# Kernel tuning notes

Hardware: AMD Instinct MI355X
Metric: run time of the kernel (lower is better)

Reference implementation:

```python
import jax, jax.numpy as jnp
import numpy as np

EPS = 1e-10
B, N, F, H, C = 4, 512, 64, 64, 32


def _lin_init(key, fan_in, fan_out):
    return jax.random.normal(key, (fan_in, fan_out), dtype=jnp.float32) / np.sqrt(fan_in)


def setup_inputs() -> dict:
    key = jax.random.key(0)
    ks = jax.random.split(key, 12)
    inp = {
        "h": jax.random.normal(ks[0], (B, N, F), dtype=jnp.float32),
        "x": jax.random.normal(ks[1], (B, N, 3), dtype=jnp.float32),
        "mask": jnp.ones((B, N, N), dtype=jnp.float32),
        # edge_model (ConcatenationFilter): Linear(2F+1,H) SiLU Linear(H,H) SiLU
        "We1": _lin_init(ks[2], 2 * F + 1, H), "be1": jnp.zeros((H,), jnp.float32),
        "We2": _lin_init(ks[3], H, H), "be2": jnp.zeros((H,), jnp.float32),
        # coefficients_mlp: Linear(H,H) SiLU Linear(H,C)
        "Wc1": _lin_init(ks[4], H, H), "bc1": jnp.zeros((H,), jnp.float32),
        "Wc2": _lin_init(ks[5], H, C), "bc2": jnp.zeros((C,), jnp.float32),
        # post_norm_mlp: Linear(C,H) SiLU Linear(H,H)
        "Wp1": _lin_init(ks[6], C, H), "bp1": jnp.zeros((H,), jnp.float32),
        "Wp2": _lin_init(ks[7], H, H), "bp2": jnp.zeros((H,), jnp.float32),
        # node_mlp: Linear(2H+F,H) SiLU Linear(H,F)
        "Wn1": _lin_init(ks[8], 2 * H + F, H), "bn1": jnp.zeros((H,), jnp.float32),
        "Wn2": _lin_init(ks[9], H, F), "bn2": jnp.zeros((F,), jnp.float32),
    }
    return inp


def _forward(h, x, mask, We1, be1, We2, be2, Wc1, bc1, Wc2, bc2,
             Wp1, bp1, Wp2, bp2, Wn1, bn1, Wn2, bn2):
    b, n, f = h.shape
    # pairwise displacements: entry (i, j) = x_j - x_i  -> [B,N,N,3]
    x_minus_xt = x[..., None, :, :] - x[..., :, None, :]
    # squared pairwise distance (norm with eps=0, then squared) -> [B,N,N,1]
    norm2 = jnp.sum(x_minus_xt * x_minus_xt, axis=-1, keepdims=True)
    # h_cat_ht: [h_i broadcast over j dim order per get_h_cat_h] -> [B,N,N,2F]
    hi = jnp.broadcast_to(h[..., None, :, :], (b, n, n, f))
    hj = jnp.broadcast_to(h[..., :, None, :], (b, n, n, f))
    edge_in = jnp.concatenate([hi, hj, norm2], axis=-1)  # [B,N,N,2F+1]
    # ConcatenationFilter edge model
    h_e_mtx = jax.nn.silu(jax.nn.silu(edge_in @ We1 + be1) @ We2 + be2)  # [B,N,N,H]
    # aggregate (masked sum over neighbor dim -2)
    h_e = jnp.sum(h_e_mtx * mask[..., None], axis=-2)  # [B,N,H]
    # spatial attention
    coeff = jax.nn.silu(h_e_mtx @ Wc1 + bc1) @ Wc2 + bc2  # [B,N,N,C]
    vec = x_minus_xt / (norm2 ** 2.0 + EPS)  # [B,N,N,3]
    # combinations = coeff[...,c,None] * vec[...,None,:]; masked sum over dim -3 (j)
    comb_sum = jnp.einsum("bijc,bijd,bij->bicd", coeff, vec, mask)  # [B,N,C,3]
    comb_norm = jnp.sum(comb_sum * comb_sum, axis=-1)  # [B,N,C]
    h_comb = jax.nn.silu(comb_norm @ Wp1 + bp1) @ Wp2 + bp2  # [B,N,H]
    # node model with residual
    node_in = jnp.concatenate([h, h_e, h_comb], axis=-1)  # [B,N,F+2H]
    out = jax.nn.silu(node_in @ Wn1 + bn1) @ Wn2 + bn2  # [B,N,F]
    h_new = h + out
    return h_new


def reference(h, x, mask, We1, be1, We2, be2, Wc1, bc1, Wc2, bc2,
              Wp1, bp1, Wp2, bp2, Wn1, bn1, Wn2, bn2):
    h_new = _forward(h, x, mask, We1, be1, We2, be2, Wc1, bc1, Wc2, bc2,
                     Wp1, bp1, Wp2, bp2, Wn1, bn1, Wn2, bn2)
    # update_coordinate=False: x passes through unchanged
    return (h_new, x)
```

## Files before the change

### kernel.cpp

```cpp
#include <hip/hip_runtime.h>

#define BB 4
#define NN 512
#define FF 64

typedef __attribute__((ext_vector_type(8))) short short8v;
typedef __attribute__((ext_vector_type(4))) float f32x4;

__device__ __forceinline__ float silu_f(float v) {
  return v * __builtin_amdgcn_rcpf(1.0f + __expf(-v));
}
__device__ __forceinline__ unsigned short f2bf(float f) {
  unsigned int u = __float_as_uint(f);
  unsigned int r = (u + 0x7FFFu + ((u >> 16) & 1u)) >> 16;
  return (unsigned short)r;
}
__device__ __forceinline__ float bf2f(unsigned short s) {
  return __uint_as_float(((unsigned int)s) << 16);
}
__device__ __forceinline__ unsigned cvt_pk_bf16(float a, float b) {
  unsigned r;
  asm("v_cvt_pk_bf16_f32 %0, %1, %2" : "=v"(r) : "v"(a), "v"(b));
  return r;
}

#define AIDX(j, k) ((((j) << 6)) | (((((k) >> 3) ^ ((j) & 7))) << 3) | ((k) & 7))

__global__ void sake_prep(const float* __restrict__ h, const float* __restrict__ We1,
                          const float* __restrict__ be1, const float* __restrict__ We2,
                          const float* __restrict__ Wc1, const float* __restrict__ Wc2,
                          float* __restrict__ G, float* __restrict__ Base,
                          unsigned short* __restrict__ w2h, unsigned short* __restrict__ w2l,
                          unsigned short* __restrict__ w3h, unsigned short* __restrict__ w3l,
                          unsigned short* __restrict__ w4h, unsigned short* __restrict__ w4l)
{
  const int wg = (int)blockIdx.x, tid = (int)threadIdx.x;
  if (wg < 64) {
    __shared__ float sH[32][64];
    const int r0 = wg * 32;
    for (int idx = tid; idx < 2048; idx += 256) sH[idx >> 6][idx & 63] = h[r0 * 64 + idx];
    __syncthreads();
    const int rl = tid >> 3;
    const int o0 = (tid & 7) * 8;
    float aG[8], aB[8];
    #pragma unroll
    for (int o = 0; o < 8; ++o) { aG[o] = 0.f; aB[o] = be1[o0 + o]; }
    for (int k = 0; k < 64; ++k) {
      const float hv = sH[rl][k];
      const float4 g0 = *(const float4*)&We1[k * 64 + o0];
      const float4 g1 = *(const float4*)&We1[k * 64 + o0 + 4];
      const float4 b0 = *(const float4*)&We1[(64 + k) * 64 + o0];
      const float4 b1 = *(const float4*)&We1[(64 + k) * 64 + o0 + 4];
      aG[0] = fmaf(hv, g0.x, aG[0]); aG[1] = fmaf(hv, g0.y, aG[1]);
      aG[2] = fmaf(hv, g0.z, aG[2]); aG[3] = fmaf(hv, g0.w, aG[3]);
      aG[4] = fmaf(hv, g1.x, aG[4]); aG[5] = fmaf(hv, g1.y, aG[5]);
      aG[6] = fmaf(hv, g1.z, aG[6]); aG[7] = fmaf(hv, g1.w, aG[7]);
      aB[0] = fmaf(hv, b0.x, aB[0]); aB[1] = fmaf(hv, b0.y, aB[1]);
      aB[2] = fmaf(hv, b0.z, aB[2]); aB[3] = fmaf(hv, b0.w, aB[3]);
      aB[4] = fmaf(hv, b1.x, aB[4]); aB[5] = fmaf(hv, b1.y, aB[5]);
      aB[6] = fmaf(hv, b1.z, aB[6]); aB[7] = fmaf(hv, b1.w, aB[7]);
    }
    const size_t base = (size_t)(r0 + rl) * 64 + o0;
    *(float4*)&G[base]        = make_float4(aG[0], aG[1], aG[2], aG[3]);
    *(float4*)&G[base + 4]    = make_float4(aG[4], aG[5], aG[6], aG[7]);
    *(float4*)&Base[base]     = make_float4(aB[0], aB[1], aB[2], aB[3]);
    *(float4*)&Base[base + 4] = make_float4(aB[4], aB[5], aB[6], aB[7]);
  } else {
    for (int idx = tid; idx < 10240; idx += 256) {
      float w; unsigned short *ph, *pl; int pos;
      if (idx < 4096)      { const int o = idx >> 6,          k = idx & 63;
                             w = We2[k * 64 + o]; ph = w2h; pl = w2l; pos = o * 64 + k; }
      else if (idx < 8192) { const int t = idx - 4096, o = t >> 6, k = t & 63;
                             w = Wc1[k * 64 + o]; ph = w3h; pl = w3l; pos = o * 64 + k; }
      else                 { const int t = idx - 8192, c = t >> 6, k = t & 63;
                             w = Wc2[k * 32 + c]; ph = w4h; pl = w4l; pos = c * 64 + k; }
      const unsigned short hi = f2bf(w);
      const unsigned short lo = f2bf(w - bf2f(hi));
      ph[pos] = hi; pl[pos] = lo;
    }
  }
}

__device__ __forceinline__ void pack_store4(unsigned short* sAh, int a,
                                            float v0, float v1, float v2, float v3) {
  *(uint2*)&sAh[a] = make_uint2(cvt_pk_bf16(v0, v1), cvt_pk_bf16(v2, v3));
}

__global__ __launch_bounds__(256, 3)
void sake_mfma(const float* __restrict__ h, const float* __restrict__ x,
               const float* __restrict__ mask,
               const float* __restrict__ We1, const float* __restrict__ be2,
               const float* __restrict__ bc1, const float* __restrict__ bc2,
               const float* __restrict__ Wp1, const float* __restrict__ bp1,
               const float* __restrict__ Wp2, const float* __restrict__ bp2,
               const float* __restrict__ Wn1, const float* __restrict__ bn1,
               const float* __restrict__ Wn2, const float* __restrict__ bn2,
               const float* __restrict__ G, const float* __restrict__ Base,
               const unsigned short* __restrict__ w2h, const unsigned short* __restrict__ w2l,
               const unsigned short* __restrict__ w3h, const unsigned short* __restrict__ w3l,
               const unsigned short* __restrict__ w4h, const unsigned short* __restrict__ w4l,
               float* __restrict__ out)
{
  __shared__ unsigned short sAh[2 * 4096];
  __shared__ float sVecM[64][4];
  __shared__ float sMask[64];
  __shared__ float sBase[64], sW1n[64], sHi[64], sXi[4];
  __shared__ float sHe[64], sCombP[4 * 48], sCN[32], sTmp[64], sHcomb[64];

  const int tid  = (int)threadIdx.x;
  const int blk  = (int)blockIdx.x;
  const int b    = blk >> 9;
  const int i    = blk & 511;
  const int lane = tid & 63;
  const int wid  = tid >> 6;
  const int l15  = lane & 15;
  const int lg   = lane >> 4;
  const int mb   = wid * 16;
  const int mb2  = (wid >> 1) * 16;

  if (tid < 64) {
    sBase[tid] = Base[((size_t)(b * NN + i)) * 64 + tid];
    sW1n[tid]  = We1[128 * 64 + tid];
    sHi[tid]   = h[((size_t)(b * NN + i)) * 64 + tid];
  }
  if (tid < 3) sXi[tid] = x[((size_t)(b * NN + i)) * 3 + tid];

  short8v w2hF[2], w2lF[2], w3hF[2], w3lF[2], w4hF[2], w4lF[2];
  #pragma unroll
  for (int ks = 0; ks < 2; ++ks) {
    const int ko = ks * 32 + lg * 8;
    w2hF[ks] = *(const short8v*)&w2h[(mb  + l15) * 64 + ko];
    w2lF[ks] = *(const short8v*)&w2l[(mb  + l15) * 64 + ko];
    w3hF[ks] = *(const short8v*)&w3h[(mb  + l15) * 64 + ko];
    w3lF[ks] = *(const short8v*)&w3l[(mb  + l15) * 64 + ko];
    w4hF[ks] = *(const short8v*)&w4h[(mb2 + l15) * 64 + ko];
    w4lF[ks] = *(const short8v*)&w4l[(mb2 + l15) * 64 + ko];
  }
  float be2v[4], bc1v[4], bc2v[4];
  #pragma unroll
  for (int r = 0; r < 4; ++r) {
    be2v[r] = be2[mb  + lg * 4 + r];
    bc1v[r] = bc1[mb  + lg * 4 + r];
    bc2v[r] = bc2[mb2 + lg * 4 + r];
  }

  float heAcc[4] = {0.f, 0.f, 0.f, 0.f};
  float cAcc[4][3] = {};

  for (int jt = 0; jt < 8; ++jt) {
    const int jb = jt * 64;
    __syncthreads();

    if (tid < 64) {
      const int j = tid;
      const size_t xo = ((size_t)(b * NN + jb + j)) * 3;
      const float dx = x[xo + 0] - sXi[0];
      const float dy = x[xo + 1] - sXi[1];
      const float dz = x[xo + 2] - sXi[2];
      const float n2 = dx * dx + dy * dy + dz * dz;
      const float inv = __builtin_amdgcn_rcpf(n2 * n2 + 1e-10f);
      const float m = mask[((size_t)(b * NN + i)) * NN + jb + j];
      sVecM[j][0] = dx * inv * m; sVecM[j][1] = dy * inv * m; sVecM[j][2] = dz * inv * m;
      sMask[j] = m;
    }

    {
      const int j = l15 + wid * 16;
      const int jglob = jb + j;
      const size_t xo = ((size_t)(b * NN + jglob)) * 3;
      const float dx = x[xo + 0] - sXi[0];
      const float dy = x[xo + 1] - sXi[1];
      const float dz = x[xo + 2] - sXi[2];
      const float n2 = dx * dx + dy * dy + dz * dz;
      #pragma unroll
      for (int kk = 0; kk < 4; ++kk) {
        const int kb = lg * 16 + kk * 4;
        const float4 g4 = *(const float4*)&G[((size_t)(b * NN + jglob)) * 64 + kb];
        const float4 bs = *(const float4*)&sBase[kb];
        const float4 wn = *(const float4*)&sW1n[kb];
        const float v0 = silu_f(g4.x + bs.x + n2 * wn.x);
        const float v1 = silu_f(g4.y + bs.y + n2 * wn.y);
        const float v2 = silu_f(g4.z + bs.z + n2 * wn.z);
        const float v3 = silu_f(g4.w + bs.w + n2 * wn.w);
        pack_store4(sAh, AIDX(j, kb), v0, v1, v2, v3);
      }
    }
    __syncthreads();

    #pragma unroll
    for (int nf = 0; nf < 4; ++nf) {
      const int jn = nf * 16 + l15;
      f32x4 acc = { be2v[0], be2v[1], be2v[2], be2v[3] };
      #pragma unroll
      for (int ks = 0; ks < 2; ++ks) {
        const int kb = ks * 32 + lg * 8;
        const short8v bh = *(const short8v*)&sAh[AIDX(jn, kb)];
        acc = __builtin_amdgcn_mfma_f32_16x16x32_bf16(w2hF[ks], bh, acc, 0, 0, 0);
        acc = __builtin_amdgcn_mfma_f32_16x16x32_bf16(w2lF[ks], bh, acc, 0, 0, 0);
      }
      const float m = sMask[jn];
      float v[4];
      #pragma unroll
      for (int r = 0; r < 4; ++r) { v[r] = silu_f(acc[r]); heAcc[r] = fmaf(v[r], m, heAcc[r]); }
      pack_store4(sAh, 4096 + AIDX(jn, mb + lg * 4), v[0], v[1], v[2], v[3]);
    }
    __syncthreads();

    #pragma unroll
    for (int nf = 0; nf < 4; ++nf) {
      const int jn = nf * 16 + l15;
      f32x4 acc = { bc1v[0], bc1v[1], bc1v[2], bc1v[3] };
      #pragma unroll
      for (int ks = 0; ks < 2; ++ks) {
        const int kb = ks * 32 + lg * 8;
        const short8v bh = *(const short8v*)&sAh[4096 + AIDX(jn, kb)];
        acc = __builtin_amdgcn_mfma_f32_16x16x32_bf16(w3hF[ks], bh, acc, 0, 0, 0);
        acc = __builtin_amdgcn_mfma_f32_16x16x32_bf16(w3lF[ks], bh, acc, 0, 0, 0);
      }
      float v[4];
      #pragma unroll
      for (int r = 0; r < 4; ++r) v[r] = silu_f(acc[r]);
      pack_store4(sAh, AIDX(jn, mb + lg * 4), v[0], v[1], v[2], v[3]);
    }
    __syncthreads();

    #pragma unroll
    for (int nf = 0; nf < 2; ++nf) {
      const int jn = (wid & 1) * 32 + nf * 16 + l15;
      f32x4 acc = { bc2v[0], bc2v[1], bc2v[2], bc2v[3] };
      #pragma unroll
      for (int ks = 0; ks < 2; ++ks) {
        const int kb = ks * 32 + lg * 8;
        const short8v bh = *(const short8v*)&sAh[AIDX(jn, kb)];
        acc = __builtin_amdgcn_mfma_f32_16x16x32_bf16(w4hF[ks], bh, acc, 0, 0, 0);
        acc = __builtin_amdgcn_mfma_f32_16x16x32_bf16(w4lF[ks], bh, acc, 0, 0, 0);
      }
      const float vm0 = sVecM[jn][0], vm1 = sVecM[jn][1], vm2 = sVecM[jn][2];
      #pragma unroll
      for (int r = 0; r < 4; ++r) {
        cAcc[r][0] = fmaf(acc[r], vm0, cAcc[r][0]);
        cAcc[r][1] = fmaf(acc[r], vm1, cAcc[r][1]);
        cAcc[r][2] = fmaf(acc[r], vm2, cAcc[r][2]);
      }
    }
  }

  #pragma unroll
  for (int r = 0; r < 4; ++r) {
    float s = heAcc[r];
    s += __shfl_xor(s, 1); s += __shfl_xor(s, 2); s += __shfl_xor(s, 4); s += __shfl_xor(s, 8);
    if (l15 == 0) sHe[mb + lg * 4 + r] = s;
  }
  #pragma unroll
  for (int r = 0; r < 4; ++r)
    #pragma unroll
    for (int d = 0; d < 3; ++d) {
      float s = cAcc[r][d];
      s += __shfl_xor(s, 1); s += __shfl_xor(s, 2); s += __shfl_xor(s, 4); s += __shfl_xor(s, 8);
      if (l15 == 0) sCombP[wid * 48 + (lg * 4 + r) * 3 + d] = s;
    }
  __syncthreads();
  if (tid < 32) {
    const int c = tid, w0 = (c >> 4) * 2, cl = c & 15;
    const float s0 = sCombP[w0 * 48 + cl * 3 + 0] + sCombP[(w0 + 1) * 48 + cl * 3 + 0];
    const float s1 = sCombP[w0 * 48 + cl * 3 + 1] + sCombP[(w0 + 1) * 48 + cl * 3 + 1];
    const float s2 = sCombP[w0 * 48 + cl * 3 + 2] + sCombP[(w0 + 1) * 48 + cl * 3 + 2];
    sCN[c] = s0 * s0 + s1 * s1 + s2 * s2;
  }
  __syncthreads();

  if (tid < 64) {
    float s = bp1[tid];
    #pragma unroll 8
    for (int c = 0; c < 32; ++c) s = fmaf(sCN[c], Wp1[c * 64 + tid], s);
    sTmp[tid] = silu_f(s);
  }
  __syncthreads();
  if (tid < 64) {
    float s = bp2[tid];
    #pragma unroll 16
    for (int k = 0; k < 64; ++k) s = fmaf(sTmp[k], Wp2[k * 64 + tid], s);
    sHcomb[tid] = s;
  }
  __syncthreads();
  if (tid < 64) {
    float s = bn1[tid];
    #pragma unroll 16
    for (int m = 0; m < 64; ++m) s = fmaf(sHi[m],    Wn1[m * 64 + tid],         s);
    #pragma unroll 16
    for (int m = 0; m < 64; ++m) s = fmaf(sHe[m],    Wn1[(64 + m) * 64 + tid],  s);
    #pragma unroll 16
    for (int m = 0; m < 64; ++m) s = fmaf(sHcomb[m], Wn1[(128 + m) * 64 + tid], s);
    sTmp[tid] = silu_f(s);
  }
  __syncthreads();
  if (tid < 64) {
    float s = bn2[tid];
    #pragma unroll 16
    for (int k = 0; k < 64; ++k) s = fmaf(sTmp[k], Wn2[k * 64 + tid], s);
    out[((size_t)(b * NN + i)) * 64 + tid] = sHi[tid] + s;
  } else if (tid < 67) {
    const int d = tid - 64;
    out[(size_t)BB * NN * FF + ((size_t)(b * NN + i)) * 3 + d] = x[((size_t)(b * NN + i)) * 3 + d];
  }
}

extern "C" void kernel_launch(void* const* d_in, const int* in_sizes, int n_in,
                              void* d_out, int out_size, void* d_ws, size_t ws_size,
                              hipStream_t stream) {
  const float* h    = (const float*)d_in[0];
  const float* x    = (const float*)d_in[1];
  const float* mask = (const float*)d_in[2];
  const float* We1  = (const float*)d_in[3];
  const float* be1  = (const float*)d_in[4];
  const float* We2  = (const float*)d_in[5];
  const float* be2  = (const float*)d_in[6];
  const float* Wc1  = (const float*)d_in[7];
  const float* bc1  = (const float*)d_in[8];
  const float* Wc2  = (const float*)d_in[9];
  const float* bc2  = (const float*)d_in[10];
  const float* Wp1  = (const float*)d_in[11];
  const float* bp1  = (const float*)d_in[12];
  const float* Wp2  = (const float*)d_in[13];
  const float* bp2  = (const float*)d_in[14];
  const float* Wn1  = (const float*)d_in[15];
  const float* bn1  = (const float*)d_in[16];
  const float* Wn2  = (const float*)d_in[17];
  const float* bn2  = (const float*)d_in[18];
  float* out = (float*)d_out;

  float* G    = (float*)d_ws;
  float* Base = G + 2048 * 64;
  unsigned short* w2h = (unsigned short*)(Base + 2048 * 64);
  unsigned short* w2l = w2h + 4096;
  unsigned short* w3h = w2l + 4096;
  unsigned short* w3l = w3h + 4096;
  unsigned short* w4h = w3l + 4096;
  unsigned short* w4l = w4h + 2048;

  hipLaunchKernelGGL(sake_prep, dim3(65), dim3(256), 0, stream,
                     h, We1, be1, We2, Wc1, Wc2, G, Base,
                     w2h, w2l, w3h, w3l, w4h, w4l);
  hipLaunchKernelGGL(sake_mfma, dim3(BB * NN), dim3(256), 0, stream,
                     h, x, mask, We1, be2, bc1, bc2,
                     Wp1, bp1, Wp2, bp2, Wn1, bn1, Wn2, bn2,
                     G, Base, w2h, w2l, w3h, w3l, w4h, w4l, out);
}
```

Baseline: 127.3 us.

## Process 128-neighbor tiles with triple-buffered LDS to cut barriers per tile

Doubles the neighbor tile from 64 to 128 (4 iterations instead of 8) and gives each MLP stage its own LDS buffer, so the loop-top barrier is dropped and there are three barriers per tile instead of four. The final coefficient layer is reorganized so each wave computes all 32 outputs for its own neighbor rows, keeping the displacement vectors in registers instead of a shared sVecM array. Biases move to shared memory. LDS use grows to about 48KB per block and register pressure rises, which may reduce occupancy under the 3-blocks-per-CU launch bound.

```diff
diff --git a/kernel.cpp b/kernel.cpp
--- a/kernel.cpp
+++ b/kernel.cpp
@@ -81,9 +81,9 @@
   }
 }
 
-__device__ __forceinline__ void pack_store4(unsigned short* sAh, int a,
+__device__ __forceinline__ void pack_store4(unsigned short* sA, int a,
                                             float v0, float v1, float v2, float v3) {
-  *(uint2*)&sAh[a] = make_uint2(cvt_pk_bf16(v0, v1), cvt_pk_bf16(v2, v3));
+  *(uint2*)&sA[a] = make_uint2(cvt_pk_bf16(v0, v1), cvt_pk_bf16(v2, v3));
 }
 
 __global__ __launch_bounds__(256, 3)
@@ -101,11 +101,11 @@
                const unsigned short* __restrict__ w4h, const unsigned short* __restrict__ w4l,
                float* __restrict__ out)
 {
-  __shared__ unsigned short sAh[2 * 4096];
-  __shared__ float sVecM[64][4];
-  __shared__ float sMask[64];
-  __shared__ float sBase[64], sW1n[64], sHi[64], sXi[4];
-  __shared__ float sHe[64], sCombP[4 * 48], sCN[32], sTmp[64], sHcomb[64];
+  __shared__ unsigned short sAct[3 * 8192];
+  __shared__ float sMaskL[128];
+  __shared__ float sBase[64], sW1n[64], sHi[64];
+  __shared__ float sB2[64], sB3[64], sB4[32];
+  __shared__ float sHe[64], sCombP[4][96], sCN[32], sTmp[64], sHcomb[64];
 
   const int tid  = (int)threadIdx.x;
   const int blk  = (int)blockIdx.x;
@@ -116,131 +116,135 @@
   const int l15  = lane & 15;
   const int lg   = lane >> 4;
   const int mb   = wid * 16;
-  const int mb2  = (wid >> 1) * 16;
 
   if (tid < 64) {
     sBase[tid] = Base[((size_t)(b * NN + i)) * 64 + tid];
     sW1n[tid]  = We1[128 * 64 + tid];
     sHi[tid]   = h[((size_t)(b * NN + i)) * 64 + tid];
-  }
-  if (tid < 3) sXi[tid] = x[((size_t)(b * NN + i)) * 3 + tid];
-
-  short8v w2hF[2], w2lF[2], w3hF[2], w3lF[2], w4hF[2], w4lF[2];
+    sB2[tid]   = be2[tid];
+    sB3[tid]   = bc1[tid];
+  }
+  if (tid < 32) sB4[tid] = bc2[tid];
+  const float xi0 = x[((size_t)(b * NN + i)) * 3 + 0];
+  const float xi1 = x[((size_t)(b * NN + i)) * 3 + 1];
+  const float xi2 = x[((size_t)(b * NN + i)) * 3 + 2];
+
+  short8v w2hF[2], w2lF[2], w3hF[2], w3lF[2], w4hF[2][2], w4lF[2][2];
   #pragma unroll
   for (int ks = 0; ks < 2; ++ks) {
     const int ko = ks * 32 + lg * 8;
-    w2hF[ks] = *(const short8v*)&w2h[(mb  + l15) * 64 + ko];
-    w2lF[ks] = *(const short8v*)&w2l[(mb  + l15) * 64 + ko];
-    w3hF[ks] = *(const short8v*)&w3h[(mb  + l15) * 64 + ko];
-    w3lF[ks] = *(const short8v*)&w3l[(mb  + l15) * 64 + ko];
-    w4hF[ks] = *(const short8v*)&w4h[(mb2 + l15) * 64 + ko];
-    w4lF[ks] = *(const short8v*)&w4l[(mb2 + l15) * 64 + ko];
-  }
-  float be2v[4], bc1v[4], bc2v[4];
-  #pragma unroll
-  for (int r = 0; r < 4; ++r) {
-    be2v[r] = be2[mb  + lg * 4 + r];
-    bc1v[r] = bc1[mb  + lg * 4 + r];
-    bc2v[r] = bc2[mb2 + lg * 4 + r];
+    w2hF[ks] = *(const short8v*)&w2h[(mb + l15) * 64 + ko];
+    w2lF[ks] = *(const short8v*)&w2l[(mb + l15) * 64 + ko];
+    w3hF[ks] = *(const short8v*)&w3h[(mb + l15) * 64 + ko];
+    w3lF[ks] = *(const short8v*)&w3l[(mb + l15) * 64 + ko];
+    #pragma unroll
+    for (int m2 = 0; m2 < 2; ++m2) {
+      w4hF[m2][ks] = *(const short8v*)&w4h[(m2 * 16 + l15) * 64 + ko];
+      w4lF[m2][ks] = *(const short8v*)&w4l[(m2 * 16 + l15) * 64 + ko];
+    }
   }
 
   float heAcc[4] = {0.f, 0.f, 0.f, 0.f};
-  float cAcc[4][3] = {};
-
-  for (int jt = 0; jt < 8; ++jt) {
-    const int jb = jt * 64;
-    __syncthreads();
-
-    if (tid < 64) {
-      const int j = tid;
-      const size_t xo = ((size_t)(b * NN + jb + j)) * 3;
-      const float dx = x[xo + 0] - sXi[0];
-      const float dy = x[xo + 1] - sXi[1];
-      const float dz = x[xo + 2] - sXi[2];
+  float cAcc[2][4][3] = {};
+
+  __syncthreads();
+
+  for (int jt = 0; jt < 4; ++jt) {
+    const int jb = jt * 128;
+
+    float vmr[2][3], n2v[2];
+    #pragma unroll
+    for (int jj = 0; jj < 2; ++jj) {
+      const int j = jb + jj * 64 + wid * 16 + l15;
+      const size_t xo = ((size_t)(b * NN + j)) * 3;
+      const float dx = x[xo + 0] - xi0;
+      const float dy = x[xo + 1] - xi1;
+      const float dz = x[xo + 2] - xi2;
       const float n2 = dx * dx + dy * dy + dz * dz;
       const float inv = __builtin_amdgcn_rcpf(n2 * n2 + 1e-10f);
-      const float m = mask[((size_t)(b * NN + i)) * NN + jb + j];
-      sVecM[j][0] = dx * inv * m; sVecM[j][1] = dy * inv * m; sVecM[j][2] = dz * inv * m;
-      sMask[j] = m;
-    }
-
-    {
-      const int j = l15 + wid * 16;
-      const int jglob = jb + j;
-      const size_t xo = ((size_t)(b * NN + jglob)) * 3;
-      const float dx = x[xo + 0] - sXi[0];
-      const float dy = x[xo + 1] - sXi[1];
-      const float dz = x[xo + 2] - sXi[2];
-      const float n2 = dx * dx + dy * dy + dz * dz;
-      #pragma unroll
-      for (int kk = 0; kk < 4; ++kk) {
-        const int kb = lg * 16 + kk * 4;
-        const float4 g4 = *(const float4*)&G[((size_t)(b * NN + jglob)) * 64 + kb];
-        const float4 bs = *(const float4*)&sBase[kb];
-        const float4 wn = *(const float4*)&sW1n[kb];
+      const float m = mask[((size_t)(b * NN + i)) * NN + j];
+      vmr[jj][0] = dx * inv * m; vmr[jj][1] = dy * inv * m; vmr[jj][2] = dz * inv * m;
+      n2v[jj] = n2;
+      if (lg == 0) sMaskL[jj * 64 + wid * 16 + l15] = m;
+    }
+    #pragma unroll
+    for (int kk = 0; kk < 4; ++kk) {
+      const int kb = lg * 16 + kk * 4;
+      const float4 bs = *(const float4*)&sBase[kb];
+      const float4 wn = *(const float4*)&sW1n[kb];
+      #pragma unroll
+      for (int jj = 0; jj < 2; ++jj) {
+        const int jloc = jj * 64 + wid * 16 + l15;
+        const float4 g4 = *(const float4*)&G[((size_t)(b * NN + jb + jloc)) * 64 + kb];
+        const float n2 = n2v[jj];
         const float v0 = silu_f(g4.x + bs.x + n2 * wn.x);
         const float v1 = silu_f(g4.y + bs.y + n2 * wn.y);
         const float v2 = silu_f(g4.z + bs.z + n2 * wn.z);
         const float v3 = silu_f(g4.w + bs.w + n2 * wn.w);
-        pack_store4(sAh, AIDX(j, kb), v0, v1, v2, v3);
+        pack_store4(sAct, AIDX(jloc, kb), v0, v1, v2, v3);
       }
     }
     __syncthreads();
 
-    #pragma unroll
-    for (int nf = 0; nf < 4; ++nf) {
-      const int jn = nf * 16 + l15;
-      f32x4 acc = { be2v[0], be2v[1], be2v[2], be2v[3] };
-      #pragma unroll
-      for (int ks = 0; ks < 2; ++ks) {
-        const int kb = ks * 32 + lg * 8;
-        const short8v bh = *(const short8v*)&sAh[AIDX(jn, kb)];
-        acc = __builtin_amdgcn_mfma_f32_16x16x32_bf16(w2hF[ks], bh, acc, 0, 0, 0);
-        acc = __builtin_amdgcn_mfma_f32_16x16x32_bf16(w2lF[ks], bh, acc, 0, 0, 0);
-      }
-      const float m = sMask[jn];
-      float v[4];
-      #pragma unroll
-      for (int r = 0; r < 4; ++r) { v[r] = silu_f(acc[r]); heAcc[r] = fmaf(v[r], m, heAcc[r]); }
-      pack_store4(sAh, 4096 + AIDX(jn, mb + lg * 4), v[0], v[1], v[2], v[3]);
+    {
+      const f32x4 bias = *(const f32x4*)&sB2[mb + lg * 4];
+      #pragma unroll
+      for (int nf = 0; nf < 8; ++nf) {
+        const int jn = nf * 16 + l15;
+        f32x4 acc = bias;
+        #pragma unroll
+        for (int ks = 0; ks < 2; ++ks) {
+          const short8v bh = *(const short8v*)&sAct[AIDX(jn, ks * 32 + lg * 8)];
+          acc = __builtin_amdgcn_mfma_f32_16x16x32_bf16(w2hF[ks], bh, acc, 0, 0, 0);
+          acc = __builtin_amdgcn_mfma_f32_16x16x32_bf16(w2lF[ks], bh, acc, 0, 0, 0);
+        }
+        const float m = sMaskL[jn];
+        float v[4];
+        #pragma unroll
+        for (int r = 0; r < 4; ++r) { v[r] = silu_f(acc[r]); heAcc[r] = fmaf(v[r], m, heAcc[r]); }
+        pack_store4(sAct, 8192 + AIDX(jn, mb + lg * 4), v[0], v[1], v[2], v[3]);
+      }
     }
     __syncthreads();
 
-    #pragma unroll
-    for (int nf = 0; nf < 4; ++nf) {
-      const int jn = nf * 16 + l15;
-      f32x4 acc = { bc1v[0], bc1v[1], bc1v[2], bc1v[3] };
-      #pragma unroll
-      for (int ks = 0; ks < 2; ++ks) {
-        const int kb = ks * 32 + lg * 8;
-        const short8v bh = *(const short8v*)&sAh[4096 + AIDX(jn, kb)];
-        acc = __builtin_amdgcn_mfma_f32_16x16x32_bf16(w3hF[ks], bh, acc, 0, 0, 0);
-        acc = __builtin_amdgcn_mfma_f32_16x16x32_bf16(w3lF[ks], bh, acc, 0, 0, 0);
-      }
-      float v[4];
-      #pragma unroll
-      for (int r = 0; r < 4; ++r) v[r] = silu_f(acc[r]);
-      pack_store4(sAh, AIDX(jn, mb + lg * 4), v[0], v[1], v[2], v[3]);
+    {
+      const f32x4 bias = *(const f32x4*)&sB3[mb + lg * 4];
+      #pragma unroll
+      for (int nf = 0; nf < 8; ++nf) {
+        const int jn = nf * 16 + l15;
+        f32x4 acc = bias;
+        #pragma unroll
+        for (int ks = 0; ks < 2; ++ks) {
+          const short8v bh = *(const short8v*)&sAct[8192 + AIDX(jn, ks * 32 + lg * 8)];
+          acc = __builtin_amdgcn_mfma_f32_16x16x32_bf16(w3hF[ks], bh, acc, 0, 0, 0);
+          acc = __builtin_amdgcn_mfma_f32_16x16x32_bf16(w3lF[ks], bh, acc, 0, 0, 0);
+        }
+        float v[4];
+        #pragma unroll
+        for (int r = 0; r < 4; ++r) v[r] = silu_f(acc[r]);
+        pack_store4(sAct, 16384 + AIDX(jn, mb + lg * 4), v[0], v[1], v[2], v[3]);
+      }
     }
     __syncthreads();
 
     #pragma unroll
-    for (int nf = 0; nf < 2; ++nf) {
-      const int jn = (wid & 1) * 32 + nf * 16 + l15;
-      f32x4 acc = { bc2v[0], bc2v[1], bc2v[2], bc2v[3] };
-      #pragma unroll
-      for (int ks = 0; ks < 2; ++ks) {
-        const int kb = ks * 32 + lg * 8;
-        const short8v bh = *(const short8v*)&sAh[AIDX(jn, kb)];
-        acc = __builtin_amdgcn_mfma_f32_16x16x32_bf16(w4hF[ks], bh, acc, 0, 0, 0);
-        acc = __builtin_amdgcn_mfma_f32_16x16x32_bf16(w4lF[ks], bh, acc, 0, 0, 0);
-      }
-      const float vm0 = sVecM[jn][0], vm1 = sVecM[jn][1], vm2 = sVecM[jn][2];
-      #pragma unroll
-      for (int r = 0; r < 4; ++r) {
-        cAcc[r][0] = fmaf(acc[r], vm0, cAcc[r][0]);
-        cAcc[r][1] = fmaf(acc[r], vm1, cAcc[r][1]);
-        cAcc[r][2] = fmaf(acc[r], vm2, cAcc[r][2]);
+    for (int jj = 0; jj < 2; ++jj) {
+      const int jloc = jj * 64 + wid * 16 + l15;
+      const short8v bh0 = *(const short8v*)&sAct[16384 + AIDX(jloc, lg * 8)];
+      const short8v bh1 = *(const short8v*)&sAct[16384 + AIDX(jloc, 32 + lg * 8)];
+      #pragma unroll
+      for (int m2 = 0; m2 < 2; ++m2) {
+        f32x4 acc = *(const f32x4*)&sB4[m2 * 16 + lg * 4];
+        acc = __builtin_amdgcn_mfma_f32_16x16x32_bf16(w4hF[m2][0], bh0, acc, 0, 0, 0);
+        acc = __builtin_amdgcn_mfma_f32_16x16x32_bf16(w4lF[m2][0], bh0, acc, 0, 0, 0);
+        acc = __builtin_amdgcn_mfma_f32_16x16x32_bf16(w4hF[m2][1], bh1, acc, 0, 0, 0);
+        acc = __builtin_amdgcn_mfma_f32_16x16x32_bf16(w4lF[m2][1], bh1, acc, 0, 0, 0);
+        #pragma unroll
+        for (int r = 0; r < 4; ++r) {
+          cAcc[m2][r][0] = fmaf(acc[r], vmr[jj][0], cAcc[m2][r][0]);
+          cAcc[m2][r][1] = fmaf(acc[r], vmr[jj][1], cAcc[m2][r][1]);
+          cAcc[m2][r][2] = fmaf(acc[r], vmr[jj][2], cAcc[m2][r][2]);
+        }
       }
     }
   }
@@ -252,19 +256,25 @@
     if (l15 == 0) sHe[mb + lg * 4 + r] = s;
   }
   #pragma unroll
-  for (int r = 0; r < 4; ++r)
-    #pragma unroll
-    for (int d = 0; d < 3; ++d) {
-      float s = cAcc[r][d];
-      s += __shfl_xor(s, 1); s += __shfl_xor(s, 2); s += __shfl_xor(s, 4); s += __shfl_xor(s, 8);
-      if (l15 == 0) sCombP[wid * 48 + (lg * 4 + r) * 3 + d] = s;
-    }
+  for (int m2 = 0; m2 < 2; ++m2)
+    #pragma unroll
+    for (int r = 0; r < 4; ++r)
+      #pragma unroll
+      for (int d = 0; d < 3; ++d) {
+        float s = cAcc[m2][r][d];
+        s += __shfl_xor(s, 1); s += __shfl_xor(s, 2); s += __shfl_xor(s, 4); s += __shfl_xor(s, 8);
+        if (l15 == 0) sCombP[wid][(m2 * 16 + lg * 4 + r) * 3 + d] = s;
+      }
   __syncthreads();
   if (tid < 32) {
-    const int c = tid, w0 = (c >> 4) * 2, cl = c & 15;
-    const float s0 = sCombP[w0 * 48 + cl * 3 + 0] + sCombP[(w0 + 1) * 48 + cl * 3 + 0];
-    const float s1 = sCombP[w0 * 48 + cl * 3 + 1] + sCombP[(w0 + 1) * 48 + cl * 3 + 1];
-    const float s2 = sCombP[w0 * 48 + cl * 3 + 2] + sCombP[(w0 + 1) * 48 + cl * 3 + 2];
+    const int c = tid;
+    float s0 = 0.f, s1 = 0.f, s2 = 0.f;
+    #pragma unroll
+    for (int w = 0; w < 4; ++w) {
+      s0 += sCombP[w][c * 3 + 0];
+      s1 += sCombP[w][c * 3 + 1];
+      s2 += sCombP[w][c * 3 + 2];
+    }
     sCN[c] = s0 * s0 + s1 * s1 + s2 * s2;
   }
   __syncthreads();
```

Result: slower. 172.5 us (+35.5%).
